# Optimization experiments

Measured on AMD Instinct MI355X. Metric: run time of the kernel, lower is better.

The kernel has to match this reference:

```python
import jax, jax.numpy as jnp
import numpy as np

B, T, D, UNITS = 16, 4096, 1024, 1024


def setup_inputs() -> dict:
    key = jax.random.key(0)
    k1, k2 = jax.random.split(key)
    inputs = jax.random.normal(k1, (B, T, D), dtype=jnp.float32)
    att_keral = jax.random.normal(k2, (UNITS, D), dtype=jnp.float32) * 0.02
    return {"inputs": inputs, "att_keral": att_keral}


def reference(inputs, att_keral):
    # scores[b,t,u] = inputs[b,t,d] * att_keral[u,d] / sqrt(D)
    d = inputs.shape[-1]
    scale = 1.0 / jnp.sqrt(jnp.asarray(d, dtype=jnp.float32))
    scores = jnp.einsum('btd,ud->btu', inputs, att_keral) * scale
    # NOTE: the original computes alpha = softmax(scores) but (for isfinal=False)
    # multiplies the *scaled scores* (not alpha) back with att_keral. We reproduce
    # that exact math (alpha is dead code on this path).
    out = jnp.einsum('btu,ud->btd', scores, att_keral)
    return out
```

## Files before the change

kernel.cpp:

```cpp
#include <hip/hip_runtime.h>


typedef unsigned short u16;
typedef unsigned int u32;
typedef __bf16 bf16x8 __attribute__((ext_vector_type(8)));
typedef float f32x4 __attribute__((ext_vector_type(4)));

#define BAR() __builtin_amdgcn_s_barrier()
#define LGKM0() asm volatile("s_waitcnt lgkmcnt(0)" ::: "memory")
#define VMC(n) asm volatile("s_waitcnt vmcnt(" #n ")" ::: "memory")
#define SCHED0() __builtin_amdgcn_sched_barrier(0)

__device__ __forceinline__ u16 f2bf(float f) {
  u32 u = __float_as_uint(f);
  u += 0x7fffu + ((u >> 16) & 1u);
  return (u16)(u >> 16);
}

__device__ __forceinline__ void gload_lds16(const void* g, void* l) {
  __builtin_amdgcn_global_load_lds((const __attribute__((address_space(1))) u32*)g,
                                   (__attribute__((address_space(3))) u32*)l,
                                   16, 0, 0);
}

__device__ __forceinline__ void load2x16(const float* p, f32x4& a, f32x4& b) {
  asm volatile("global_load_dwordx4 %0, %2, off\n\t"
               "global_load_dwordx4 %1, %2, off offset:16"
               : "=&v"(a), "=&v"(b)
               : "v"(p)
               : "memory");
}

__device__ __forceinline__ bf16x8 cvt8(f32x4 a, f32x4 b) {
  bf16x8 h;
  h[0] = (__bf16)a[0]; h[1] = (__bf16)a[1]; h[2] = (__bf16)a[2]; h[3] = (__bf16)a[3];
  h[4] = (__bf16)b[0]; h[5] = (__bf16)b[1]; h[6] = (__bf16)b[2]; h[7] = (__bf16)b[3];
  return h;
}

__global__ __launch_bounds__(256) void compute_M(const float* __restrict__ W,
                                                 u16* __restrict__ Mb) {
  __shared__ float w1[32][64];
  __shared__ float w2[32][64];
  const int t = threadIdx.x;
  const int i0 = blockIdx.y * 64;
  const int j0 = blockIdx.x * 64;
  const int tx = t & 15, ty = t >> 4;
  float acc[4][4] = {};
  for (int u0 = 0; u0 < 1024; u0 += 32) {
    __syncthreads();
#pragma unroll
    for (int p = 0; p < 2; ++p) {
      int idx = p * 256 + t;
      int lu = idx >> 4, lc = (idx & 15) * 4;
      *(float4*)&w1[lu][lc] = *(const float4*)(W + (size_t)(u0 + lu) * 1024 + i0 + lc);
      *(float4*)&w2[lu][lc] = *(const float4*)(W + (size_t)(u0 + lu) * 1024 + j0 + lc);
    }
    __syncthreads();
#pragma unroll 8
    for (int u = 0; u < 32; ++u) {
      float4 a = *(const float4*)&w1[u][ty * 4];
      float4 b = *(const float4*)&w2[u][tx * 4];
      float av[4] = {a.x, a.y, a.z, a.w};
      float bv[4] = {b.x, b.y, b.z, b.w};
#pragma unroll
      for (int e = 0; e < 4; ++e)
#pragma unroll
        for (int f = 0; f < 4; ++f)
          acc[e][f] += av[e] * bv[f];
    }
  }
  const float s = 0.03125f;
#pragma unroll
  for (int e = 0; e < 4; ++e) {
    ushort4 v;
    v.x = f2bf(acc[e][0] * s);
    v.y = f2bf(acc[e][1] * s);
    v.z = f2bf(acc[e][2] * s);
    v.w = f2bf(acc[e][3] * s);
    *(ushort4*)(Mb + (size_t)(i0 + ty * 4 + e) * 1024 + j0 + tx * 4) = v;
  }
}

__global__ __launch_bounds__(512, 2) void gemm8f(const float* __restrict__ X,
                                                 const u16* __restrict__ Mb,
                                                 float* __restrict__ out) {
  __shared__ u16 lA[4][8192];
  __shared__ u16 lB[4][8192];

  const int p = blockIdx.x;
  const int wg = (p & 7) * 128 + (p >> 3);
  const int bm = wg >> 2;
  const int bn = wg & 3;
  const size_t r0 = (size_t)bm * 256;
  const int c0 = bn * 256;

  const int t = threadIdx.x;
  const int lane = t & 63;
  const int w = t >> 6;
  const int wr = w >> 2, wc = w & 3;
  const int fr = lane & 15;
  const int kc = lane >> 4;

  const int srow = t >> 2;
  const int scl = t & 3;
  const int csw = scl ^ ((srow >> 1) & 3);
  const float* aLo = X + (r0 + srow) * 1024 + scl * 8;
  const float* aHi = X + (r0 + 128 + srow) * 1024 + scl * 8;
  u16* wLo = &lA[0][srow * 32 + csw * 8];
  u16* wHi = &lA[0][(srow + 128) * 32 + csw * 8];
  const int scg = csw;
  const u16* gB0 = Mb + (size_t)(c0 + srow) * 1024 + scg * 8;
  const u16* gB1 = Mb + (size_t)(c0 + 128 + srow) * 1024 + scg * 8;
  const int sl0 = w * 512;
  const int sl1 = 4096 + w * 512;

  f32x4 acc[8][4] = {};
  f32x4 q0a, q0b, q0c, q0d, q1a, q1b, q1c, q1d, q2a, q2b, q2c, q2d;
  f32x4 pfa, pfb, pfc, pfd;

  load2x16(aLo + 0 * 32, q0a, q0b);  load2x16(aHi + 0 * 32, q0c, q0d);
  load2x16(aLo + 1 * 32, q1a, q1b);  load2x16(aHi + 1 * 32, q1c, q1d);
  load2x16(aLo + 2 * 32, q2a, q2b);  load2x16(aHi + 2 * 32, q2c, q2d);
#pragma unroll
  for (int jt = 0; jt < 3; ++jt) {
    gload_lds16(gB0 + jt * 32, (void*)&lB[jt][sl0]);
    gload_lds16(gB1 + jt * 32, (void*)&lB[jt][sl1]);
  }
  load2x16(aLo + 3 * 32, pfa, pfb);  load2x16(aHi + 3 * 32, pfc, pfd);
  VMC(8);
  SCHED0();
  *(bf16x8*)(wLo + 0 * 8192) = cvt8(q0a, q0b);
  *(bf16x8*)(wHi + 0 * 8192) = cvt8(q0c, q0d);
  *(bf16x8*)(wLo + 1 * 8192) = cvt8(q1a, q1b);
  *(bf16x8*)(wHi + 1 * 8192) = cvt8(q1c, q1d);
  *(bf16x8*)(wLo + 2 * 8192) = cvt8(q2a, q2b);
  *(bf16x8*)(wHi + 2 * 8192) = cvt8(q2c, q2d);
  LGKM0();
  BAR();

  for (int j = 0; j < 32; ++j) {
    const int rb = j & 3;
    const int sb = (j + 3) & 3;
    const u16* bA = &lA[rb][0];
    const u16* bB = &lB[rb][0];

    if (j == 0 || j == 30) { VMC(0); } else { VMC(2); }
    SCHED0();
    if (j <= 28) {
      *(bf16x8*)(wLo + sb * 8192) = cvt8(pfa, pfb);
      *(bf16x8*)(wHi + sb * 8192) = cvt8(pfc, pfd);
    }
    bf16x8 af[4], bf[4];
#pragma unroll
    for (int m = 0; m < 4; ++m) {
      const int row = wr * 128 + m * 16 + fr;
      const int cs = kc ^ ((row >> 1) & 3);
      af[m] = *(const bf16x8*)&bA[row * 32 + cs * 8];
    }
#pragma unroll
    for (int n = 0; n < 4; ++n) {
      const int row = wc * 64 + n * 16 + fr;
      const int cs = kc ^ ((row >> 1) & 3);
      bf[n] = *(const bf16x8*)&bB[row * 32 + cs * 8];
    }
    if (j <= 27) {
      load2x16(aLo + (j + 4) * 32, pfa, pfb);
      load2x16(aHi + (j + 4) * 32, pfc, pfd);
    }
    BAR();
    LGKM0();
    __builtin_amdgcn_s_setprio(1);
#pragma unroll
    for (int m = 0; m < 4; ++m)
#pragma unroll
      for (int n = 0; n < 4; ++n)
        acc[m][n] = __builtin_amdgcn_mfma_f32_16x16x32_bf16(af[m], bf[n],
                                                            acc[m][n], 0, 0, 0);
    __builtin_amdgcn_s_setprio(0);
    BAR();
#pragma unroll
    for (int m = 0; m < 4; ++m) {
      const int row = wr * 128 + (m + 4) * 16 + fr;
      const int cs = kc ^ ((row >> 1) & 3);
      af[m] = *(const bf16x8*)&bA[row * 32 + cs * 8];
    }
    if (j <= 28) {
      gload_lds16(gB0 + (j + 3) * 32, (void*)&lB[sb][sl0]);
      gload_lds16(gB1 + (j + 3) * 32, (void*)&lB[sb][sl1]);
    }
    BAR();
    LGKM0();
    __builtin_amdgcn_s_setprio(1);
#pragma unroll
    for (int m = 0; m < 4; ++m)
#pragma unroll
      for (int n = 0; n < 4; ++n)
        acc[m + 4][n] = __builtin_amdgcn_mfma_f32_16x16x32_bf16(af[m], bf[n],
                                                                acc[m + 4][n], 0, 0, 0);
    __builtin_amdgcn_s_setprio(0);
    BAR();
  }

  const int ocol = lane & 15;
  const int orow = (lane >> 4) * 4;
#pragma unroll
  for (int m = 0; m < 8; ++m) {
    const size_t rbase = (r0 + wr * 128 + m * 16 + orow) * 1024;
#pragma unroll
    for (int n = 0; n < 4; ++n) {
      float* o = out + rbase + (c0 + wc * 64 + n * 16 + ocol);
      o[0] = acc[m][n][0];
      o[1024] = acc[m][n][1];
      o[2048] = acc[m][n][2];
      o[3072] = acc[m][n][3];
    }
  }
}

extern "C" void kernel_launch(void* const* d_in, const int* in_sizes, int n_in,
                              void* d_out, int out_size, void* d_ws, size_t ws_size,
                              hipStream_t stream) {
  const float* X = (const float*)d_in[0];
  const float* W = (const float*)d_in[1];
  float* out = (float*)d_out;
  u16* Mb = (u16*)d_ws;

  compute_M<<<dim3(16, 16), 256, 0, stream>>>(W, Mb);
  gemm8f<<<1024, 512, 0, stream>>>(X, Mb, out);
}
```

Measured before the change: 264.9 us.

## Shrink GEMM tile to 256x128, cut pipeline depth, raise occupancy to four blocks

The main GEMM tile goes from 256x256 to 256x128 and the grid doubles to 2048 workgroups. The A operand buffering drops from four stages to two, and B uses a three-stage ring. Accumulator registers are halved and launch bounds now ask for four blocks per CU, trading prefetch depth and per-block data reuse for more concurrent waves to hide latency. Each A row tile is now converted from fp32 twice (once per column block), which raises global read traffic for X.

```diff
diff --git a/kernel.cpp b/kernel.cpp
--- a/kernel.cpp
+++ b/kernel.cpp
@@ -82,23 +82,23 @@
   }
 }
 
-__global__ __launch_bounds__(512, 2) void gemm8f(const float* __restrict__ X,
-                                                 const u16* __restrict__ Mb,
-                                                 float* __restrict__ out) {
-  __shared__ u16 lA[4][8192];
-  __shared__ u16 lB[4][8192];
+__global__ __launch_bounds__(512, 4) void gemm_xm(const float* __restrict__ X,
+                                                  const u16* __restrict__ Mb,
+                                                  float* __restrict__ out) {
+  __shared__ u16 lA[2][8192];
+  __shared__ u16 lB[3][4096];
 
   const int p = blockIdx.x;
-  const int wg = (p & 7) * 128 + (p >> 3);
-  const int bm = wg >> 2;
-  const int bn = wg & 3;
+  const int wg = (p & 7) * 256 + (p >> 3);
+  const int bm = wg >> 3;
+  const int bn = wg & 7;
   const size_t r0 = (size_t)bm * 256;
-  const int c0 = bn * 256;
+  const int c0 = bn * 128;
 
   const int t = threadIdx.x;
   const int lane = t & 63;
   const int w = t >> 6;
-  const int wr = w >> 2, wc = w & 3;
+  const int wr = w >> 1, wc = w & 1;
   const int fr = lane & 15;
   const int kc = lane >> 4;
 
@@ -109,52 +109,42 @@
   const float* aHi = X + (r0 + 128 + srow) * 1024 + scl * 8;
   u16* wLo = &lA[0][srow * 32 + csw * 8];
   u16* wHi = &lA[0][(srow + 128) * 32 + csw * 8];
-  const int scg = csw;
-  const u16* gB0 = Mb + (size_t)(c0 + srow) * 1024 + scg * 8;
-  const u16* gB1 = Mb + (size_t)(c0 + 128 + srow) * 1024 + scg * 8;
-  const int sl0 = w * 512;
-  const int sl1 = 4096 + w * 512;
-
-  f32x4 acc[8][4] = {};
-  f32x4 q0a, q0b, q0c, q0d, q1a, q1b, q1c, q1d, q2a, q2b, q2c, q2d;
+  const u16* gB = Mb + (size_t)(c0 + srow) * 1024 + csw * 8;
+  const int slB = w * 512;
+
+  f32x4 acc[4][4] = {};
   f32x4 pfa, pfb, pfc, pfd;
-
-  load2x16(aLo + 0 * 32, q0a, q0b);  load2x16(aHi + 0 * 32, q0c, q0d);
-  load2x16(aLo + 1 * 32, q1a, q1b);  load2x16(aHi + 1 * 32, q1c, q1d);
-  load2x16(aLo + 2 * 32, q2a, q2b);  load2x16(aHi + 2 * 32, q2c, q2d);
-#pragma unroll
-  for (int jt = 0; jt < 3; ++jt) {
-    gload_lds16(gB0 + jt * 32, (void*)&lB[jt][sl0]);
-    gload_lds16(gB1 + jt * 32, (void*)&lB[jt][sl1]);
-  }
-  load2x16(aLo + 3 * 32, pfa, pfb);  load2x16(aHi + 3 * 32, pfc, pfd);
-  VMC(8);
+  f32x4 q0a, q0b, q0c, q0d;
+
+  load2x16(aLo, q0a, q0b);
+  load2x16(aHi, q0c, q0d);
+  load2x16(aLo + 32, pfa, pfb);
+  load2x16(aHi + 32, pfc, pfd);
+  gload_lds16(gB, (void*)&lB[0][slB]);
+  gload_lds16(gB + 32, (void*)&lB[1][slB]);
+  VMC(1);
   SCHED0();
-  *(bf16x8*)(wLo + 0 * 8192) = cvt8(q0a, q0b);
-  *(bf16x8*)(wHi + 0 * 8192) = cvt8(q0c, q0d);
-  *(bf16x8*)(wLo + 1 * 8192) = cvt8(q1a, q1b);
-  *(bf16x8*)(wHi + 1 * 8192) = cvt8(q1c, q1d);
-  *(bf16x8*)(wLo + 2 * 8192) = cvt8(q2a, q2b);
-  *(bf16x8*)(wHi + 2 * 8192) = cvt8(q2c, q2d);
+  *(bf16x8*)(wLo) = cvt8(q0a, q0b);
+  *(bf16x8*)(wHi) = cvt8(q0c, q0d);
   LGKM0();
   BAR();
 
+  int rbB = 0, wbB = 2;
   for (int j = 0; j < 32; ++j) {
-    const int rb = j & 3;
-    const int sb = (j + 3) & 3;
-    const u16* bA = &lA[rb][0];
-    const u16* bB = &lB[rb][0];
-
-    if (j == 0 || j == 30) { VMC(0); } else { VMC(2); }
+    const u16* bA = &lA[j & 1][0];
+    const u16* bB = &lB[rbB][0];
+
+    VMC(1);
     SCHED0();
-    if (j <= 28) {
-      *(bf16x8*)(wLo + sb * 8192) = cvt8(pfa, pfb);
-      *(bf16x8*)(wHi + sb * 8192) = cvt8(pfc, pfd);
+    if (j <= 30) {
+      const int ab = ((j + 1) & 1) * 8192;
+      *(bf16x8*)(wLo + ab) = cvt8(pfa, pfb);
+      *(bf16x8*)(wHi + ab) = cvt8(pfc, pfd);
     }
     bf16x8 af[4], bf[4];
 #pragma unroll
     for (int m = 0; m < 4; ++m) {
-      const int row = wr * 128 + m * 16 + fr;
+      const int row = wr * 64 + m * 16 + fr;
       const int cs = kc ^ ((row >> 1) & 3);
       af[m] = *(const bf16x8*)&bA[row * 32 + cs * 8];
     }
@@ -164,12 +154,14 @@
       const int cs = kc ^ ((row >> 1) & 3);
       bf[n] = *(const bf16x8*)&bB[row * 32 + cs * 8];
     }
-    if (j <= 27) {
-      load2x16(aLo + (j + 4) * 32, pfa, pfb);
-      load2x16(aHi + (j + 4) * 32, pfc, pfd);
+    if (j <= 29) {
+      load2x16(aLo + (j + 2) * 32, pfa, pfb);
+      load2x16(aHi + (j + 2) * 32, pfc, pfd);
+      gload_lds16(gB + (j + 2) * 32, (void*)&lB[wbB][slB]);
     }
     BAR();
     LGKM0();
+    SCHED0();
     __builtin_amdgcn_s_setprio(1);
 #pragma unroll
     for (int m = 0; m < 4; ++m)
@@ -178,35 +170,22 @@
         acc[m][n] = __builtin_amdgcn_mfma_f32_16x16x32_bf16(af[m], bf[n],
                                                             acc[m][n], 0, 0, 0);
     __builtin_amdgcn_s_setprio(0);
+    if (j <= 29) {
+      VMC(5);
+    } else if (j == 30) {
+      VMC(0);
+    }
+    SCHED0();
     BAR();
-#pragma unroll
-    for (int m = 0; m < 4; ++m) {
-      const int row = wr * 128 + (m + 4) * 16 + fr;
-      const int cs = kc ^ ((row >> 1) & 3);
-      af[m] = *(const bf16x8*)&bA[row * 32 + cs * 8];
-    }
-    if (j <= 28) {
-      gload_lds16(gB0 + (j + 3) * 32, (void*)&lB[sb][sl0]);
-      gload_lds16(gB1 + (j + 3) * 32, (void*)&lB[sb][sl1]);
-    }
-    BAR();
-    LGKM0();
-    __builtin_amdgcn_s_setprio(1);
-#pragma unroll
-    for (int m = 0; m < 4; ++m)
-#pragma unroll
-      for (int n = 0; n < 4; ++n)
-        acc[m + 4][n] = __builtin_amdgcn_mfma_f32_16x16x32_bf16(af[m], bf[n],
-                                                                acc[m + 4][n], 0, 0, 0);
-    __builtin_amdgcn_s_setprio(0);
-    BAR();
+    rbB = (rbB == 2) ? 0 : rbB + 1;
+    wbB = (wbB == 2) ? 0 : wbB + 1;
   }
 
   const int ocol = lane & 15;
   const int orow = (lane >> 4) * 4;
 #pragma unroll
-  for (int m = 0; m < 8; ++m) {
-    const size_t rbase = (r0 + wr * 128 + m * 16 + orow) * 1024;
+  for (int m = 0; m < 4; ++m) {
+    const size_t rbase = (r0 + wr * 64 + m * 16 + orow) * 1024;
 #pragma unroll
     for (int n = 0; n < 4; ++n) {
       float* o = out + rbase + (c0 + wc * 64 + n * 16 + ocol);
@@ -227,5 +206,5 @@
   u16* Mb = (u16*)d_ws;
 
   compute_M<<<dim3(16, 16), 256, 0, stream>>>(W, Mb);
-  gemm8f<<<1024, 512, 0, stream>>>(X, Mb, out);
-}
+  gemm_xm<<<2048, 512, 0, stream>>>(X, Mb, out);
+}
```

Result: slower. 307.9 us (+16.2%).
